# Optimization experiments

Measured on AMD Instinct MI355X. Metric: run time of the kernel, lower is better.

## Reference

```python
import jax, jax.numpy as jnp
import numpy as np

N_PILLARS_X = 512
N_PILLARS_Y = 512
IN_FEATURES = 6
OUT_FEATURES = 64
N_POINTS = 1_000_000
BN_EPS = 1e-5


def setup_inputs() -> dict:
    key = jax.random.key(0)
    k_x, k_idx, k_w, k_b, k_g, k_beta = jax.random.split(key, 6)
    x = jax.random.normal(k_x, (N_POINTS, IN_FEATURES), dtype=jnp.float32)
    indices = jax.random.randint(k_idx, (N_POINTS, 2), 0, N_PILLARS_X, dtype=jnp.int32)
    # Linear params (torch default init: U(-1/sqrt(fan_in), 1/sqrt(fan_in)))
    bound = 1.0 / np.sqrt(IN_FEATURES)
    W = jax.random.uniform(k_w, (OUT_FEATURES, IN_FEATURES), jnp.float32, -bound, bound)
    b = jax.random.uniform(k_b, (OUT_FEATURES,), jnp.float32, -bound, bound)
    # BatchNorm affine params (torch default: gamma=1, beta=0; randomize slightly)
    gamma = jnp.ones((OUT_FEATURES,), jnp.float32) + 0.1 * jax.random.normal(k_g, (OUT_FEATURES,), jnp.float32)
    beta = 0.1 * jax.random.normal(k_beta, (OUT_FEATURES,), jnp.float32)
    return {"x": x, "indices": indices, "W": W, "b": b, "gamma": gamma, "beta": beta}


def reference(x, indices, W, b, gamma, beta):
    # Linear: (N, 6) @ (6, 64) + b -> (N, 64)
    h = x @ W.T + b
    # BatchNorm1d in training mode: batch statistics over the point dimension (biased var)
    mean = jnp.mean(h, axis=0)
    var = jnp.mean(jnp.square(h - mean), axis=0)
    h = (h - mean) * (gamma * jax.lax.rsqrt(var + BN_EPS)) + beta
    # ReLU
    h = jnp.maximum(h, 0.0)
    # Scatter-add each point's feature vector into its pillar cell
    flat_idx = indices[:, 0].astype(jnp.int32) * N_PILLARS_Y + indices[:, 1].astype(jnp.int32)
    grid = jax.ops.segment_sum(h, flat_idx, num_segments=N_PILLARS_X * N_PILLARS_Y)
    return grid.reshape(N_PILLARS_X, N_PILLARS_Y, OUT_FEATURES)
```

## Files before the change

kernel.cpp:

```cpp
#include <hip/hip_runtime.h>
#include <hip/hip_fp16.h>

#define N_PY 512
#define IN_F 6
#define OUT_F 64
#define N_CELLS (512 * 512)
#define NCOARSE 256
#define NBUCKET 4096
#define N_SB (NBUCKET * 4)
#define CHUNK 2048
#define BN_EPS 1e-5


__device__ __forceinline__ unsigned pack2h(float a, float b) {
    __half ha = __float2half_rn(a), hb = __float2half_rn(b);
    unsigned short ua = *reinterpret_cast<unsigned short*>(&ha);
    unsigned short ub = *reinterpret_cast<unsigned short*>(&hb);
    return (unsigned)ua | ((unsigned)ub << 16);
}

__device__ __forceinline__ float2 unpack2h(unsigned u) {
    __half2 h = *reinterpret_cast<__half2*>(&u);
    return __half22float2(h);
}

__global__ void __launch_bounds__(256)
pfn_hist_kernel(const int* __restrict__ idx, int n, int* __restrict__ histC) {
    __shared__ int lhist[NCOARSE];
    const int tid = blockIdx.x * blockDim.x + threadIdx.x;
    const int stride = gridDim.x * blockDim.x;
    const int npairs = n >> 1;

    lhist[threadIdx.x] = 0;
    __syncthreads();

    for (int q = tid; q < npairs; q += stride) {
        const int4 ij2 = ((const int4*)idx)[q];
        atomicAdd(&lhist[(ij2.x * N_PY + ij2.y) >> 10], 1);
        atomicAdd(&lhist[(ij2.z * N_PY + ij2.w) >> 10], 1);
    }
    if ((n & 1) && tid == 0) {
        const int2 ij = ((const int2*)idx)[n - 1];
        atomicAdd(&lhist[(ij.x * N_PY + ij.y) >> 10], 1);
    }
    __syncthreads();
    atomicAdd(&histC[threadIdx.x], lhist[threadIdx.x]);
}

__global__ void __launch_bounds__(256)
pfn_scan_kernel(const int* __restrict__ histC,
                int* __restrict__ baseC, int* __restrict__ curC,
                int* __restrict__ S, int n) {
    const int tid = threadIdx.x;
    const int v = histC[tid];
    __shared__ int sc[256];
    sc[tid] = v;
    __syncthreads();
#pragma unroll
    for (int off = 1; off < 256; off <<= 1) {
        const int add = (tid >= off) ? sc[tid - off] : 0;
        __syncthreads();
        sc[tid] += add;
        __syncthreads();
    }
    const int excl = sc[tid] - v;
    baseC[tid] = excl;
    curC[tid] = excl;
    if (tid == 0) S[N_SB] = n;
}

__global__ void __launch_bounds__(256)
pfn_passA_kernel(const float* __restrict__ x, const int* __restrict__ idx,
                 int* __restrict__ curC, uint4* __restrict__ rec,
                 float* __restrict__ acc, int n) {
    __shared__ int lhist[NCOARSE];
    __shared__ int lbase[NCOARSE];
    __shared__ int lcur[NCOARSE];
    __shared__ int gbase[NCOARSE];
    __shared__ int sc[256];
    __shared__ uint4 stg[CHUNK];
    __shared__ float lmom[4][27];

    const int tid = threadIdx.x;
    const int chunkStart = blockIdx.x * CHUNK;
    const int chunkCount = min(CHUNK, n - chunkStart);

    lhist[tid] = 0;
    __syncthreads();

    float s[27];
#pragma unroll
    for (int k = 0; k < 27; ++k) s[k] = 0.f;

    int cellr[8];
    unsigned u0[8], u1[8], u2[8];
#pragma unroll
    for (int r = 0; r < 8; ++r) {
        const int i = r * 256 + tid;
        cellr[r] = -1;
        if (i < chunkCount) {
            const int p = chunkStart + i;
            const int2 ij = ((const int2*)idx)[p];
            const int cell = ij.x * N_PY + ij.y;
            cellr[r] = cell;
            const float2* xp = (const float2*)(x + (size_t)p * 6);
            const float2 a = xp[0], b2 = xp[1], c = xp[2];
            const float v6[6] = {a.x, a.y, b2.x, b2.y, c.x, c.y};
#pragma unroll
            for (int j = 0; j < 6; ++j) s[j] += v6[j];
            int k = 6;
#pragma unroll
            for (int i2 = 0; i2 < 6; ++i2)
#pragma unroll
                for (int j = i2; j < 6; ++j) { s[k] += v6[i2] * v6[j]; ++k; }
            u0[r] = pack2h(a.x, a.y);
            u1[r] = pack2h(b2.x, b2.y);
            u2[r] = pack2h(c.x, c.y);
            atomicAdd(&lhist[cell >> 10], 1);
        }
    }
    __syncthreads();

    const int v = lhist[tid];
    sc[tid] = v;
    __syncthreads();
#pragma unroll
    for (int off = 1; off < 256; off <<= 1) {
        const int add = (tid >= off) ? sc[tid - off] : 0;
        __syncthreads();
        sc[tid] += add;
        __syncthreads();
    }
    const int excl = sc[tid] - v;
    lbase[tid] = excl;
    lcur[tid] = excl;
    gbase[tid] = (v > 0) ? atomicAdd(&curC[tid], v) : 0;
    __syncthreads();

#pragma unroll
    for (int r = 0; r < 8; ++r) {
        const int cell = cellr[r];
        if (cell >= 0) {
            const int slot = atomicAdd(&lcur[cell >> 10], 1);
            stg[slot] = uint4{u0[r], u1[r], u2[r], (unsigned)cell};
        }
    }
    __syncthreads();

#pragma unroll
    for (int r = 0; r < 8; ++r) {
        const int slot = r * 256 + tid;
        if (slot < chunkCount) {
            const uint4 q = stg[slot];
            const int bkt = (int)(q.w >> 10);
            const int dst = gbase[bkt] + (slot - lbase[bkt]);
            rec[dst] = q;
        }
    }

#pragma unroll
    for (int off = 32; off > 0; off >>= 1)
#pragma unroll
        for (int k = 0; k < 27; ++k) s[k] += __shfl_down(s[k], off, 64);
    const int wid = tid >> 6;
    const int lane = tid & 63;
    if (lane == 0)
#pragma unroll
        for (int k = 0; k < 27; ++k) lmom[wid][k] = s[k];
    __syncthreads();
    if (tid < 27) {
        const int k = tid;
        atomicAdd(&acc[k], lmom[0][k] + lmom[1][k] + lmom[2][k] + lmom[3][k]);
    }
}

__global__ void __launch_bounds__(256)
pfn_passB_kernel(const uint4* __restrict__ rec, uint4* __restrict__ rec2,
                 const int* __restrict__ baseC, const int* __restrict__ histC,
                 int* __restrict__ S, int n,
                 const float* __restrict__ acc,
                 const float* __restrict__ W,
                 const float* __restrict__ b,
                 const float* __restrict__ gamma,
                 const float* __restrict__ beta,
                 float* __restrict__ Wp, float* __restrict__ bp) {
    __shared__ int lh[64];
    __shared__ int lc[64];
    const int tid = threadIdx.x;
    const int c = blockIdx.x;
    const int segbase = baseC[c];
    const int cnt = histC[c];

    if (tid < 64) lh[tid] = 0;
    __syncthreads();

    if (c == 0 && tid < 64) {
        const int f = tid;
        double inv_n = 1.0 / (double)n;
        double mx[6];
#pragma unroll
        for (int j = 0; j < 6; ++j) mx[j] = (double)acc[j] * inv_n;
        double C[6][6];
        {
            int k = 0;
            for (int i = 0; i < 6; ++i)
                for (int j = i; j < 6; ++j) {
                    double e = (double)acc[6 + k] * inv_n - mx[i] * mx[j];
                    C[i][j] = e; C[j][i] = e; ++k;
                }
        }
        double w[6];
#pragma unroll
        for (int j = 0; j < 6; ++j) w[j] = (double)W[f * 6 + j];
        double mean_h = (double)b[f];
#pragma unroll
        for (int j = 0; j < 6; ++j) mean_h += w[j] * mx[j];
        double var_h = 0.0;
        for (int i = 0; i < 6; ++i) {
            double tt = 0.0;
            for (int j = 0; j < 6; ++j) tt += C[i][j] * w[j];
            var_h += w[i] * tt;
        }
        double sgn = (double)gamma[f] / sqrt(var_h + BN_EPS);
#pragma unroll
        for (int j = 0; j < 6; ++j) Wp[f * 6 + j] = (float)(w[j] * sgn);
        bp[f] = (float)(((double)b[f] - mean_h) * sgn + (double)beta[f]);
    }

    for (int i = tid; i < cnt; i += 256) {
        const uint4 q = rec[segbase + i];
        const int fine = (int)((((q.w >> 6) & 15) << 2) | (q.w & 3));
        atomicAdd(&lh[fine], 1);
    }
    __syncthreads();

    if (tid < 64) {
        const int v = lh[tid];
        int incl = v;
#pragma unroll
        for (int off = 1; off < 64; off <<= 1) {
            const int t2 = __shfl_up(incl, off, 64);
            if (tid >= off) incl += t2;
        }
        const int excl = incl - v;
        lc[tid] = excl;
        S[c * 64 + tid] = segbase + excl;
    }
    __syncthreads();

    for (int i = tid; i < cnt; i += 256) {
        const uint4 q = rec[segbase + i];
        const int fine = (int)((((q.w >> 6) & 15) << 2) | (q.w & 3));
        const int off = atomicAdd(&lc[fine], 1);
        rec2[segbase + off] = q;
    }
}

__global__ void __launch_bounds__(256)
pfn_tile_kernel(const uint4* __restrict__ rec2, const int* __restrict__ S,
                const float* __restrict__ Wp, const float* __restrict__ bp,
                float* __restrict__ out) {
    __shared__ float tile[64 * OUT_F];
    __shared__ uint4 stage[4][64];
    const int tid = threadIdx.x;
    const int lane = tid & 63;
    const int wid = tid >> 6;
    const int bucket = blockIdx.x;

    float4* t4 = (float4*)tile;
#pragma unroll
    for (int i = 0; i < 4; ++i)
        t4[tid + 256 * i] = float4{0.f, 0.f, 0.f, 0.f};

    const float w0 = Wp[lane * 6 + 0];
    const float w1 = Wp[lane * 6 + 1];
    const float w2 = Wp[lane * 6 + 2];
    const float w3 = Wp[lane * 6 + 3];
    const float w4 = Wp[lane * 6 + 4];
    const float w5 = Wp[lane * 6 + 5];
    const float bb = bp[lane];

    __syncthreads();

    const int sb = (bucket << 2) | wid;
    const int r0 = S[sb];
    const int cnt = S[sb + 1] - r0;
    uint4* stg = stage[wid];

    for (int chunk = 0; chunk < cnt; chunk += 64) {
        const int m = min(64, cnt - chunk);
        const uint4* src = rec2 + (size_t)(r0 + chunk);
        if (lane < m) stg[lane] = src[lane];
#pragma unroll 4
        for (int j = 0; j < m; ++j) {
            const uint4 q = stg[j];
            const float2 f01 = unpack2h(q.x);
            const float2 f23 = unpack2h(q.y);
            const float2 f45 = unpack2h(q.z);
            float v = bb;
            v = fmaf(w0, f01.x, v); v = fmaf(w1, f01.y, v);
            v = fmaf(w2, f23.x, v); v = fmaf(w3, f23.y, v);
            v = fmaf(w4, f45.x, v); v = fmaf(w5, f45.y, v);
            tile[(((int)q.w & 63) << 6) | lane] += fmaxf(v, 0.f);
        }
    }
    __syncthreads();

    float4* o4 = (float4*)(out + (size_t)bucket * (64 * OUT_F));
#pragma unroll
    for (int i = 0; i < 4; ++i)
        o4[tid + 256 * i] = t4[tid + 256 * i];
}

__global__ void __launch_bounds__(256)
pfn_moments_kernel(const float* __restrict__ x, int n, float* __restrict__ acc) {
    const int tid = blockIdx.x * blockDim.x + threadIdx.x;
    const int stride = gridDim.x * blockDim.x;
    const int npairs = n >> 1;

    float s[27];
#pragma unroll
    for (int k = 0; k < 27; ++k) s[k] = 0.f;

    for (int q = tid; q < npairs; q += stride) {
        const float4* base4 = (const float4*)(x + (size_t)q * 12);
        const float4 a = base4[0];
        const float4 b4 = base4[1];
        const float4 c4 = base4[2];
        const float p0[6] = {a.x, a.y, a.z, a.w, b4.x, b4.y};
        const float p1[6] = {b4.z, b4.w, c4.x, c4.y, c4.z, c4.w};
#pragma unroll
        for (int j = 0; j < 6; ++j) s[j] += p0[j] + p1[j];
        int k = 6;
#pragma unroll
        for (int i = 0; i < 6; ++i)
#pragma unroll
            for (int j = i; j < 6; ++j) {
                s[k] += p0[i] * p0[j] + p1[i] * p1[j];
                ++k;
            }
    }
    if ((n & 1) && tid == 0) {
        const float* p = x + (size_t)(n - 1) * 6;
        float v[6];
#pragma unroll
        for (int j = 0; j < 6; ++j) v[j] = p[j];
#pragma unroll
        for (int j = 0; j < 6; ++j) s[j] += v[j];
        int k = 6;
#pragma unroll
        for (int i = 0; i < 6; ++i)
#pragma unroll
            for (int j = i; j < 6; ++j) { s[k] += v[i] * v[j]; ++k; }
    }

#pragma unroll
    for (int off = 32; off > 0; off >>= 1)
#pragma unroll
        for (int k = 0; k < 27; ++k) s[k] += __shfl_down(s[k], off, 64);

    __shared__ float lds[4][27];
    const int wid = threadIdx.x >> 6;
    const int lane = threadIdx.x & 63;
    if (lane == 0)
#pragma unroll
        for (int k = 0; k < 27; ++k) lds[wid][k] = s[k];
    __syncthreads();

    if (threadIdx.x < 27) {
        const int k = threadIdx.x;
        atomicAdd(&acc[k], lds[0][k] + lds[1][k] + lds[2][k] + lds[3][k]);
    }
}

__global__ void pfn_finalize_kernel(const float* __restrict__ acc,
                                    const float* __restrict__ W,
                                    const float* __restrict__ b,
                                    const float* __restrict__ gamma,
                                    const float* __restrict__ beta,
                                    int n,
                                    float* __restrict__ Wp,
                                    float* __restrict__ bp) {
    int f = threadIdx.x;
    double inv_n = 1.0 / (double)n;
    double mx[6];
#pragma unroll
    for (int j = 0; j < 6; ++j) mx[j] = (double)acc[j] * inv_n;
    double C[6][6];
    {
        int k = 0;
        for (int i = 0; i < 6; ++i)
            for (int j = i; j < 6; ++j) {
                double e = (double)acc[6 + k] * inv_n - mx[i] * mx[j];
                C[i][j] = e; C[j][i] = e; ++k;
            }
    }
    double w[6];
#pragma unroll
    for (int j = 0; j < 6; ++j) w[j] = (double)W[f * 6 + j];
    double mean_h = (double)b[f];
#pragma unroll
    for (int j = 0; j < 6; ++j) mean_h += w[j] * mx[j];
    double var_h = 0.0;
    for (int i = 0; i < 6; ++i) {
        double t = 0.0;
        for (int j = 0; j < 6; ++j) t += C[i][j] * w[j];
        var_h += w[i] * t;
    }
    double s = (double)gamma[f] / sqrt(var_h + BN_EPS);
#pragma unroll
    for (int j = 0; j < 6; ++j) Wp[f * 6 + j] = (float)(w[j] * s);
    bp[f] = (float)(((double)b[f] - mean_h) * s + (double)beta[f]);
}

__global__ void __launch_bounds__(256)
pfn_build_kernel(const int* __restrict__ idx, int n,
                 int* __restrict__ head, int* __restrict__ nxt) {
    const int p = blockIdx.x * blockDim.x + threadIdx.x;
    if (p >= n) return;
    const int2 ij = ((const int2*)idx)[p];
    const int cell = ij.x * N_PY + ij.y;
    nxt[p] = atomicExch(&head[cell], p);
}

__global__ void __launch_bounds__(256)
pfn_output_kernel(const float* __restrict__ x,
                  const int* __restrict__ head,
                  const int* __restrict__ nxt,
                  const float* __restrict__ Wp,
                  const float* __restrict__ bp,
                  float* __restrict__ out) {
    const int lane = threadIdx.x & 63;
    const int cell = __builtin_amdgcn_readfirstlane(
        (int)((blockIdx.x * blockDim.x + threadIdx.x) >> 6));

    const float w0 = Wp[lane * 6 + 0];
    const float w1 = Wp[lane * 6 + 1];
    const float w2 = Wp[lane * 6 + 2];
    const float w3 = Wp[lane * 6 + 3];
    const float w4 = Wp[lane * 6 + 4];
    const float w5 = Wp[lane * 6 + 5];
    const float bb = bp[lane];

    float s = 0.f;
    int p = head[cell];
    while (p >= 0) {
        const float* xp = x + (size_t)p * 6;
        const int pn = nxt[p];
        float v = bb;
        v = fmaf(w0, xp[0], v);
        v = fmaf(w1, xp[1], v);
        v = fmaf(w2, xp[2], v);
        v = fmaf(w3, xp[3], v);
        v = fmaf(w4, xp[4], v);
        v = fmaf(w5, xp[5], v);
        s += fmaxf(v, 0.0f);
        p = pn;
    }
    out[(size_t)cell * OUT_F + lane] = s;
}

extern "C" void kernel_launch(void* const* d_in, const int* in_sizes, int n_in,
                              void* d_out, int out_size, void* d_ws, size_t ws_size,
                              hipStream_t stream) {
    const float* x     = (const float*)d_in[0];
    const int*   idx   = (const int*)d_in[1];
    const float* W     = (const float*)d_in[2];
    const float* b     = (const float*)d_in[3];
    const float* gamma = (const float*)d_in[4];
    const float* beta  = (const float*)d_in[5];
    float* out = (float*)d_out;

    const int n = in_sizes[0] / IN_F;

    float* acc = (float*)d_ws;
    float* Wp  = (float*)((char*)d_ws + 512);
    float* bp  = Wp + OUT_F * IN_F;

    int*   histC = (int*)((char*)d_ws + 4096);
    int*   baseC = (int*)((char*)d_ws + 5120);
    int*   curC  = (int*)((char*)d_ws + 6144);
    int*   S     = (int*)((char*)d_ws + 7168);
    uint4* rec   = (uint4*)((char*)d_ws + 73728);
    uint4* rec2  = rec + n;

    const size_t need = 73728 + (size_t)n * 32;

    if (ws_size >= need) {
        hipMemsetAsync(d_ws, 0, 5120, stream);
        pfn_hist_kernel<<<256, 256, 0, stream>>>(idx, n, histC);
        pfn_scan_kernel<<<1, 256, 0, stream>>>(histC, baseC, curC, S, n);
        pfn_passA_kernel<<<(n + CHUNK - 1) / CHUNK, 256, 0, stream>>>(
            x, idx, curC, rec, acc, n);
        pfn_passB_kernel<<<NCOARSE, 256, 0, stream>>>(
            rec, rec2, baseC, histC, S, n, acc, W, b, gamma, beta, Wp, bp);
        pfn_tile_kernel<<<NBUCKET, 256, 0, stream>>>(rec2, S, Wp, bp, out);
    } else {
        int* head = (int*)((char*)d_ws + 4096);
        int* nxt  = head + N_CELLS;
        hipMemsetAsync(d_ws, 0, 512, stream);
        pfn_moments_kernel<<<1024, 256, 0, stream>>>(x, n, acc);
        hipMemsetAsync(head, 0xFF, (size_t)N_CELLS * sizeof(int), stream);
        pfn_finalize_kernel<<<1, 64, 0, stream>>>(acc, W, b, gamma, beta, n, Wp, bp);
        pfn_build_kernel<<<(n + 255) / 256, 256, 0, stream>>>(idx, n, head, nxt);
        pfn_output_kernel<<<N_CELLS / 4, 256, 0, stream>>>(x, head, nxt, Wp, bp, out);
    }
}
```

Baseline: 86.73 us.

## Compute fine-bucket histogram up front to drop passB counting pass

The histogram kernel now counts all 16K fine buckets directly with global atomics instead of 256 coarse buckets in shared memory. A single 1024-thread scan then produces all fine offsets, so passB no longer re-reads its records to build a local histogram and scatters in a single pass. This removes one full read of the record array in passB, at the cost of contended global atomics in the histogram kernel and a larger memset and scan.

```diff
diff --git a/kernel.cpp b/kernel.cpp
--- a/kernel.cpp
+++ b/kernel.cpp
@@ -12,6 +12,10 @@
 #define BN_EPS 1e-5
 
 
+__device__ __forceinline__ int fine_id(int cell) {
+    return ((cell >> 6) << 2) | (cell & 3);
+}
+
 __device__ __forceinline__ unsigned pack2h(float a, float b) {
     __half ha = __float2half_rn(a), hb = __float2half_rn(b);
     unsigned short ua = *reinterpret_cast<unsigned short*>(&ha);
@@ -25,48 +29,56 @@
 }
 
 __global__ void __launch_bounds__(256)
-pfn_hist_kernel(const int* __restrict__ idx, int n, int* __restrict__ histC) {
-    __shared__ int lhist[NCOARSE];
+pfn_hist16_kernel(const int* __restrict__ idx, int n, int* __restrict__ H16) {
     const int tid = blockIdx.x * blockDim.x + threadIdx.x;
     const int stride = gridDim.x * blockDim.x;
     const int npairs = n >> 1;
 
-    lhist[threadIdx.x] = 0;
-    __syncthreads();
-
     for (int q = tid; q < npairs; q += stride) {
         const int4 ij2 = ((const int4*)idx)[q];
-        atomicAdd(&lhist[(ij2.x * N_PY + ij2.y) >> 10], 1);
-        atomicAdd(&lhist[(ij2.z * N_PY + ij2.w) >> 10], 1);
+        atomicAdd(&H16[fine_id(ij2.x * N_PY + ij2.y)], 1);
+        atomicAdd(&H16[fine_id(ij2.z * N_PY + ij2.w)], 1);
     }
     if ((n & 1) && tid == 0) {
         const int2 ij = ((const int2*)idx)[n - 1];
-        atomicAdd(&lhist[(ij.x * N_PY + ij.y) >> 10], 1);
-    }
-    __syncthreads();
-    atomicAdd(&histC[threadIdx.x], lhist[threadIdx.x]);
-}
-
-__global__ void __launch_bounds__(256)
-pfn_scan_kernel(const int* __restrict__ histC,
-                int* __restrict__ baseC, int* __restrict__ curC,
-                int* __restrict__ S, int n) {
+        atomicAdd(&H16[fine_id(ij.x * N_PY + ij.y)], 1);
+    }
+}
+
+__global__ void __launch_bounds__(1024)
+pfn_scan16_kernel(const int* __restrict__ H16, int* __restrict__ S,
+                  int* __restrict__ curC, int n) {
     const int tid = threadIdx.x;
-    const int v = histC[tid];
-    __shared__ int sc[256];
-    sc[tid] = v;
-    __syncthreads();
-#pragma unroll
-    for (int off = 1; off < 256; off <<= 1) {
+    int v[16];
+    const int4* h4 = (const int4*)(H16 + tid * 16);
+#pragma unroll
+    for (int g = 0; g < 4; ++g) {
+        const int4 q = h4[g];
+        v[g * 4 + 0] = q.x; v[g * 4 + 1] = q.y;
+        v[g * 4 + 2] = q.z; v[g * 4 + 3] = q.w;
+    }
+    int pre[16];
+    int tot = 0;
+#pragma unroll
+    for (int k = 0; k < 16; ++k) { pre[k] = tot; tot += v[k]; }
+
+    __shared__ int sc[1024];
+    sc[tid] = tot;
+    __syncthreads();
+#pragma unroll
+    for (int off = 1; off < 1024; off <<= 1) {
         const int add = (tid >= off) ? sc[tid - off] : 0;
         __syncthreads();
         sc[tid] += add;
         __syncthreads();
     }
-    const int excl = sc[tid] - v;
-    baseC[tid] = excl;
-    curC[tid] = excl;
-    if (tid == 0) S[N_SB] = n;
+    const int excl = sc[tid] - tot;
+#pragma unroll
+    for (int k = 0; k < 16; ++k)
+        S[tid * 16 + k] = excl + pre[k];
+    if (tid == 1023) S[N_SB] = n;
+    __syncthreads();
+    if (tid < NCOARSE) curC[tid] = S[tid * 64];
 }
 
 __global__ void __launch_bounds__(256)
@@ -176,26 +188,23 @@
 
 __global__ void __launch_bounds__(256)
 pfn_passB_kernel(const uint4* __restrict__ rec, uint4* __restrict__ rec2,
-                 const int* __restrict__ baseC, const int* __restrict__ histC,
-                 int* __restrict__ S, int n,
+                 const int* __restrict__ S, int n,
                  const float* __restrict__ acc,
                  const float* __restrict__ W,
                  const float* __restrict__ b,
                  const float* __restrict__ gamma,
                  const float* __restrict__ beta,
                  float* __restrict__ Wp, float* __restrict__ bp) {
-    __shared__ int lh[64];
     __shared__ int lc[64];
     const int tid = threadIdx.x;
     const int c = blockIdx.x;
-    const int segbase = baseC[c];
-    const int cnt = histC[c];
-
-    if (tid < 64) lh[tid] = 0;
-    __syncthreads();
-
-    if (c == 0 && tid < 64) {
-        const int f = tid;
+    const int segbase = S[c * 64];
+    const int cnt = S[(c + 1) * 64] - segbase;
+
+    if (tid < 64) lc[tid] = S[c * 64 + tid];
+
+    if (c == 0 && tid >= 64 && tid < 128) {
+        const int f = tid - 64;
         double inv_n = 1.0 / (double)n;
         double mx[6];
 #pragma unroll
@@ -226,33 +235,13 @@
         for (int j = 0; j < 6; ++j) Wp[f * 6 + j] = (float)(w[j] * sgn);
         bp[f] = (float)(((double)b[f] - mean_h) * sgn + (double)beta[f]);
     }
+    __syncthreads();
 
     for (int i = tid; i < cnt; i += 256) {
         const uint4 q = rec[segbase + i];
         const int fine = (int)((((q.w >> 6) & 15) << 2) | (q.w & 3));
-        atomicAdd(&lh[fine], 1);
-    }
-    __syncthreads();
-
-    if (tid < 64) {
-        const int v = lh[tid];
-        int incl = v;
-#pragma unroll
-        for (int off = 1; off < 64; off <<= 1) {
-            const int t2 = __shfl_up(incl, off, 64);
-            if (tid >= off) incl += t2;
-        }
-        const int excl = incl - v;
-        lc[tid] = excl;
-        S[c * 64 + tid] = segbase + excl;
-    }
-    __syncthreads();
-
-    for (int i = tid; i < cnt; i += 256) {
-        const uint4 q = rec[segbase + i];
-        const int fine = (int)((((q.w >> 6) & 15) << 2) | (q.w & 3));
-        const int off = atomicAdd(&lc[fine], 1);
-        rec2[segbase + off] = q;
+        const int pos = atomicAdd(&lc[fine], 1);
+        rec2[pos] = q;
     }
 }
 
@@ -477,23 +466,22 @@
     float* Wp  = (float*)((char*)d_ws + 512);
     float* bp  = Wp + OUT_F * IN_F;
 
-    int*   histC = (int*)((char*)d_ws + 4096);
-    int*   baseC = (int*)((char*)d_ws + 5120);
-    int*   curC  = (int*)((char*)d_ws + 6144);
-    int*   S     = (int*)((char*)d_ws + 7168);
-    uint4* rec   = (uint4*)((char*)d_ws + 73728);
-    uint4* rec2  = rec + n;
-
-    const size_t need = 73728 + (size_t)n * 32;
+    int*   H16  = (int*)((char*)d_ws + 4096);
+    int*   S    = (int*)((char*)d_ws + 69632);
+    int*   curC = (int*)((char*)d_ws + 135680);
+    uint4* rec  = (uint4*)((char*)d_ws + 139264);
+    uint4* rec2 = rec + n;
+
+    const size_t need = 139264 + (size_t)n * 32;
 
     if (ws_size >= need) {
-        hipMemsetAsync(d_ws, 0, 5120, stream);
-        pfn_hist_kernel<<<256, 256, 0, stream>>>(idx, n, histC);
-        pfn_scan_kernel<<<1, 256, 0, stream>>>(histC, baseC, curC, S, n);
+        hipMemsetAsync(d_ws, 0, 69632, stream);
+        pfn_hist16_kernel<<<1024, 256, 0, stream>>>(idx, n, H16);
+        pfn_scan16_kernel<<<1, 1024, 0, stream>>>(H16, S, curC, n);
         pfn_passA_kernel<<<(n + CHUNK - 1) / CHUNK, 256, 0, stream>>>(
             x, idx, curC, rec, acc, n);
         pfn_passB_kernel<<<NCOARSE, 256, 0, stream>>>(
-            rec, rec2, baseC, histC, S, n, acc, W, b, gamma, beta, Wp, bp);
+            rec, rec2, S, n, acc, W, b, gamma, beta, Wp, bp);
         pfn_tile_kernel<<<NBUCKET, 256, 0, stream>>>(rec2, S, Wp, bp, out);
     } else {
         int* head = (int*)((char*)d_ws + 4096);
```

After: 117.5 us. 1.35x slower.
